# Optimization experiments

Hardware: AMD Instinct MI355X
Metric: run time of the kernel (lower is better)

Reference implementation:

```python
import jax, jax.numpy as jnp
import numpy as np

N_NODES = 50000
N_EDGES = 800000
F_IN = 128
HID = 128
F_EDGE = 16
F_TAB = 16
N_CLASSES = 3
BN_EPS = 1e-5


def setup_inputs() -> dict:
    key = jax.random.key(0)
    ks = jax.random.split(key, 20)
    s = lambda *sh: 1.0 / np.sqrt(sh[0])
    inp = {
        "x": jax.random.normal(ks[0], (N_NODES, F_IN), jnp.float32),
        "edge_index": jax.random.randint(ks[1], (2, N_EDGES), 0, N_NODES, jnp.int32),
        "edge_attr": jax.random.normal(ks[2], (N_EDGES, F_EDGE), jnp.float32),
        "tabular_features": jax.random.normal(ks[3], (N_EDGES, F_TAB), jnp.float32),
        # SAGEConv1: lin_l (aggregated neighbors, with bias) + lin_r (root, no bias)
        "W1l": jax.random.normal(ks[4], (F_IN, HID), jnp.float32) * s(F_IN),
        "b1l": jnp.zeros((HID,), jnp.float32),
        "W1r": jax.random.normal(ks[5], (F_IN, HID), jnp.float32) * s(F_IN),
        # SAGEConv2
        "W2l": jax.random.normal(ks[6], (HID, HID), jnp.float32) * s(HID),
        "b2l": jnp.zeros((HID,), jnp.float32),
        "W2r": jax.random.normal(ks[7], (HID, HID), jnp.float32) * s(HID),
        # BatchNorm params / running stats (eval mode)
        "g1": jnp.ones((HID,), jnp.float32), "be1": jnp.zeros((HID,), jnp.float32),
        "m1": jnp.zeros((HID,), jnp.float32), "v1": jnp.ones((HID,), jnp.float32),
        "g2": jnp.ones((HID,), jnp.float32), "be2": jnp.zeros((HID,), jnp.float32),
        "m2": jnp.zeros((HID,), jnp.float32), "v2": jnp.ones((HID,), jnp.float32),
        # Classifier MLP: (2*HID + F_EDGE + F_TAB) -> 128 -> 64 -> 3
        "Wc1": jax.random.normal(ks[8], (2 * HID + F_EDGE + F_TAB, 128), jnp.float32) * s(2 * HID + F_EDGE + F_TAB),
        "bc1": jnp.zeros((128,), jnp.float32),
        "Wc2": jax.random.normal(ks[9], (128, 64), jnp.float32) * s(128),
        "bc2": jnp.zeros((64,), jnp.float32),
        "Wc3": jax.random.normal(ks[10], (64, N_CLASSES), jnp.float32) * s(64),
        "bc3": jnp.zeros((N_CLASSES,), jnp.float32),
    }
    return inp


def _sage(x, src, dst, Wl, bl, Wr):
    # PyG SAGEConv (mean aggr): out_i = lin_l(mean_{j->i} x_j) + lin_r(x_i)
    msg = x[src]                                            # [E, F] gather
    agg = jax.ops.segment_sum(msg, dst, num_segments=N_NODES)
    cnt = jax.ops.segment_sum(jnp.ones((src.shape[0],), x.dtype), dst, num_segments=N_NODES)
    agg = agg / jnp.maximum(cnt, 1.0)[:, None]
    return agg @ Wl + bl + x @ Wr


def _bn(h, g, b, m, v):
    return (h - m) * (g * jax.lax.rsqrt(v + BN_EPS)) + b


def reference(x, edge_index, edge_attr, tabular_features,
              W1l, b1l, W1r, W2l, b2l, W2r,
              g1, be1, m1, v1, g2, be2, m2, v2,
              Wc1, bc1, Wc2, bc2, Wc3, bc3):
    src, dst = edge_index[0], edge_index[1]
    h = jax.nn.relu(_bn(_sage(x, src, dst, W1l, b1l, W1r), g1, be1, m1, v1))
    h = jax.nn.relu(_bn(_sage(h, src, dst, W2l, b2l, W2r), g2, be2, m2, v2))
    # eval mode: dropout is identity
    edge_repr = jnp.concatenate([h[src], h[dst], edge_attr, tabular_features], axis=-1)  # [E, 288]
    z = jax.nn.relu(edge_repr @ Wc1 + bc1)
    z = jax.nn.relu(z @ Wc2 + bc2)
    return z @ Wc3 + bc3  # [E, num_classes]
```

## Files before the change

### kernel.cpp

```cpp
#include <hip/hip_runtime.h>
#include <stdint.h>

#define NHID 128
#define EPB 64
#define RP  296
#define Z1P 136
#define Z2P 72

typedef _Float16 half8 __attribute__((ext_vector_type(8)));
typedef _Float16 half4v __attribute__((ext_vector_type(4)));
typedef float f32x4 __attribute__((ext_vector_type(4)));

__global__ void zero_kernel(float* __restrict__ p, size_t n4) {
    size_t i = (size_t)blockIdx.x * blockDim.x + threadIdx.x;
    size_t stride = (size_t)gridDim.x * blockDim.x;
    float4* p4 = (float4*)p;
    float4 z = make_float4(0.f, 0.f, 0.f, 0.f);
    for (size_t j = i; j < n4; j += stride) p4[j] = z;
}

__global__ void cast_f32_f16(const float* __restrict__ in, _Float16* __restrict__ outp,
                             int n8) {
    int i = blockIdx.x * 256 + threadIdx.x;
    int stride = gridDim.x * 256;
    for (int j = i; j < n8; j += stride) {
        float4 a = ((const float4*)in)[2 * j];
        float4 b = ((const float4*)in)[2 * j + 1];
        half8 v;
        v[0] = (_Float16)a.x; v[1] = (_Float16)a.y; v[2] = (_Float16)a.z; v[3] = (_Float16)a.w;
        v[4] = (_Float16)b.x; v[5] = (_Float16)b.y; v[6] = (_Float16)b.z; v[7] = (_Float16)b.w;
        ((half8*)outp)[j] = v;
    }
}

__global__ void prep_weights(const float* __restrict__ Wc1, const float* __restrict__ Wc2,
                             const float* __restrict__ Wc3,
                             const float* __restrict__ W1l, const float* __restrict__ W1r,
                             const float* __restrict__ W2l, const float* __restrict__ W2r,
                             _Float16* __restrict__ W1T, _Float16* __restrict__ W2T,
                             _Float16* __restrict__ W3T,
                             _Float16* __restrict__ WT1, _Float16* __restrict__ WT2) {
    int tid = blockIdx.x * 256 + threadIdx.x;
    if (tid < 288 * 128) {
        int n = tid / 288, k = tid % 288;
        W1T[tid] = (_Float16)Wc1[(size_t)k * 128 + n];
    }
    if (tid < 64 * 128) {
        int n = tid / 128, k = tid % 128;
        W2T[tid] = (_Float16)Wc2[(size_t)k * 64 + n];
    }
    if (tid < 16 * 64) {
        int n = tid / 64, k = tid % 64;
        W3T[tid] = (n < 3) ? (_Float16)Wc3[(size_t)k * 3 + n] : (_Float16)0.f;
    }
    if (tid < 128 * 256) {
        int n = tid / 256, k = tid % 256;
        WT1[tid] = (k < 128) ? (_Float16)W1l[(size_t)k * 128 + n]
                             : (_Float16)W1r[(size_t)(k - 128) * 128 + n];
        WT2[tid] = (k < 128) ? (_Float16)W2l[(size_t)k * 128 + n]
                             : (_Float16)W2r[(size_t)(k - 128) * 128 + n];
    }
}

__global__ void count_kernel(const int* __restrict__ dst, int* __restrict__ deg, int E) {
    int e = blockIdx.x * 256 + threadIdx.x;
    if (e < E) atomicAdd(&deg[dst[e]], 1);
}

__global__ __launch_bounds__(256) void csr_reduce(const int* __restrict__ deg,
                                                  int* __restrict__ bsum, int N) {
    __shared__ int b[256];
    int t = threadIdx.x;
    int i = blockIdx.x * 256 + t;
    int v = (i < N) ? deg[i] : 0;
    b[t] = v;
    __syncthreads();
#pragma unroll
    for (int off = 128; off > 0; off >>= 1) {
        if (t < off) b[t] += b[t + off];
        __syncthreads();
    }
    if (t == 0) bsum[blockIdx.x] = b[0];
}

__global__ __launch_bounds__(256) void csr_scan_partials(const int* __restrict__ bsum,
                                                         int* __restrict__ bpre,
                                                         int* __restrict__ rowptr,
                                                         int nb, int N) {
    __shared__ int b[256];
    int t = threadIdx.x;
    int v = (t < nb) ? bsum[t] : 0;
    b[t] = v;
    __syncthreads();
    int x = v;
#pragma unroll
    for (int off = 1; off < 256; off <<= 1) {
        int y = (t >= off) ? b[t - off] : 0;
        __syncthreads();
        x += y;
        b[t] = x;
        __syncthreads();
    }
    if (t < nb) bpre[t] = x - v;
    if (t == nb - 1) rowptr[N] = x;
}

__global__ __launch_bounds__(256) void csr_emit(const int* __restrict__ deg,
                                                const int* __restrict__ bpre,
                                                int* __restrict__ rowptr,
                                                int* __restrict__ cursor, int N) {
    __shared__ int b[256];
    int t = threadIdx.x;
    int i = blockIdx.x * 256 + t;
    int v = (i < N) ? deg[i] : 0;
    b[t] = v;
    __syncthreads();
    int x = v;
#pragma unroll
    for (int off = 1; off < 256; off <<= 1) {
        int y = (t >= off) ? b[t - off] : 0;
        __syncthreads();
        x += y;
        b[t] = x;
        __syncthreads();
    }
    if (i < N) {
        int excl = bpre[blockIdx.x] + x - v;
        rowptr[i] = excl;
        cursor[i] = excl;
    }
}

__global__ void fill_kernel(const int* __restrict__ src, const int* __restrict__ dst,
                            int* __restrict__ cursor, int* __restrict__ ssrc, int E) {
    int e = blockIdx.x * 256 + threadIdx.x;
    if (e < E) {
        int p = atomicAdd(&cursor[dst[e]], 1);
        ssrc[p] = src[e];
    }
}

__global__ __launch_bounds__(512) void sage_layer(
    const _Float16* __restrict__ xin, const int* __restrict__ rowptr,
    const int* __restrict__ ssrc,
    const _Float16* __restrict__ WT, const float* __restrict__ bl,
    const float* __restrict__ gam, const float* __restrict__ bet,
    const float* __restrict__ mu, const float* __restrict__ var,
    _Float16* __restrict__ outp, int N) {
    __shared__ _Float16 sAX[16][264];
    int tid = threadIdx.x;
    int node0 = blockIdx.x * 16;

    {
        int i = tid >> 5;
        int q = tid & 31;
        int node = node0 + i;
        int rs = rowptr[node], re = rowptr[node + 1];
        float4 acc = make_float4(0.f, 0.f, 0.f, 0.f);
        int e = rs;
        for (; e + 4 <= re; e += 4) {
            int s0 = ssrc[e], s1 = ssrc[e + 1], s2 = ssrc[e + 2], s3 = ssrc[e + 3];
            half4v v0 = *(const half4v*)&xin[(size_t)s0 * NHID + q * 4];
            half4v v1 = *(const half4v*)&xin[(size_t)s1 * NHID + q * 4];
            half4v v2 = *(const half4v*)&xin[(size_t)s2 * NHID + q * 4];
            half4v v3 = *(const half4v*)&xin[(size_t)s3 * NHID + q * 4];
            acc.x += ((float)v0[0] + (float)v1[0]) + ((float)v2[0] + (float)v3[0]);
            acc.y += ((float)v0[1] + (float)v1[1]) + ((float)v2[1] + (float)v3[1]);
            acc.z += ((float)v0[2] + (float)v1[2]) + ((float)v2[2] + (float)v3[2]);
            acc.w += ((float)v0[3] + (float)v1[3]) + ((float)v2[3] + (float)v3[3]);
        }
        for (; e < re; e++) {
            half4v v = *(const half4v*)&xin[(size_t)ssrc[e] * NHID + q * 4];
            acc.x += (float)v[0]; acc.y += (float)v[1];
            acc.z += (float)v[2]; acc.w += (float)v[3];
        }
        int deg = re - rs;
        float inv = (deg > 0) ? (1.0f / (float)deg) : 0.f;
        half4v av;
        av[0] = (_Float16)(acc.x * inv); av[1] = (_Float16)(acc.y * inv);
        av[2] = (_Float16)(acc.z * inv); av[3] = (_Float16)(acc.w * inv);
        *(half4v*)&sAX[i][q * 4] = av;
        *(half4v*)&sAX[i][128 + q * 4] = *(const half4v*)&xin[(size_t)node * NHID + q * 4];
    }
    __syncthreads();

    {
        int lane = tid & 63;
        int wave = tid >> 6;
        int l15 = lane & 15;
        int g = lane >> 4;
        const _Float16* wb = WT + (size_t)(wave * 16 + l15) * 256 + g * 8;
        f32x4 acc = (f32x4){0.f, 0.f, 0.f, 0.f};
#pragma unroll
        for (int kt = 0; kt < 8; kt++) {
            half8 af = *(const half8*)&sAX[l15][kt * 32 + g * 8];
            half8 bf = *(const half8*)(wb + kt * 32);
            acc = __builtin_amdgcn_mfma_f32_16x16x32_f16(af, bf, acc, 0, 0, 0);
        }
        int o = wave * 16 + l15;
        float scale = gam[o] * rsqrtf(var[o] + 1e-5f);
        float bias = bet[o];
        float mean = mu[o];
        float bb = bl[o];
#pragma unroll
        for (int r = 0; r < 4; r++) {
            float hv = acc[r] + bb;
            hv = (hv - mean) * scale + bias;
            hv = fmaxf(hv, 0.f);
            outp[(size_t)(node0 + g * 4 + r) * NHID + o] = (_Float16)hv;
        }
    }
}

__global__ __launch_bounds__(256, 1) void classifier_mfma(
    const _Float16* __restrict__ h2f, const int* __restrict__ src,
    const int* __restrict__ dst,
    const float* __restrict__ attr, const float* __restrict__ tab,
    const _Float16* __restrict__ W1T, const float* __restrict__ bc1,
    const _Float16* __restrict__ W2T, const float* __restrict__ bc2,
    const _Float16* __restrict__ W3T, const float* __restrict__ bc3,
    float* __restrict__ out, int E, int ntiles) {
    __shared__ _Float16 repr[EPB][RP];
    __shared__ _Float16 z1s[EPB][Z1P];
    _Float16* z2f = &repr[0][0];

    int tid = threadIdx.x;
    int lane = tid & 63;
    int wave = tid >> 6;
    int l15 = lane & 15;
    int g = lane >> 4;

    half8 B1[2][9];
#pragma unroll
    for (int nn = 0; nn < 2; nn++) {
        const _Float16* wb = W1T + (size_t)((2 * wave + nn) * 16 + l15) * 288 + g * 8;
#pragma unroll
        for (int kt = 0; kt < 9; kt++) B1[nn][kt] = *(const half8*)(wb + kt * 32);
    }
    float bias1[2];
#pragma unroll
    for (int nn = 0; nn < 2; nn++) bias1[nn] = bc1[(2 * wave + nn) * 16 + l15];
    half8 B2[4];
    const _Float16* w2base = W2T + (size_t)(wave * 16 + l15) * 128 + g * 8;
#pragma unroll
    for (int kt = 0; kt < 4; kt++) B2[kt] = *(const half8*)(w2base + kt * 32);
    float bias2 = bc2[wave * 16 + l15];
    half8 B3[2];
#pragma unroll
    for (int kt = 0; kt < 2; kt++)
        B3[kt] = *(const half8*)(W3T + (size_t)l15 * 64 + kt * 32 + g * 8);
    float bias3 = bc3[l15 < 3 ? l15 : 2];

    for (int t = blockIdx.x; t < ntiles; t += gridDim.x) {
        int e0 = t * EPB;
        {
            int el = tid >> 2, p = tid & 3;
            int e = e0 + el; if (e >= E) e = E - 1;
            int s = src[e], d = dst[e];
            const half8* hs = (const half8*)(h2f + (size_t)s * NHID + p * 32);
            const half8* hd = (const half8*)(h2f + (size_t)d * NHID + p * 32);
            half8* r = (half8*)&repr[el][0];
#pragma unroll
            for (int j = 0; j < 4; j++) r[p * 4 + j] = hs[j];
#pragma unroll
            for (int j = 0; j < 4; j++) r[16 + p * 4 + j] = hd[j];
            const float* ssrcp = (p < 2) ? (attr + (size_t)e * 16 + p * 8)
                                         : (tab + (size_t)e * 16 + (p - 2) * 8);
            int doff = (p < 2) ? (32 + p) : (34 + (p - 2));
            float4 a = ((const float4*)ssrcp)[0], b = ((const float4*)ssrcp)[1];
            half8 v;
            v[0] = (_Float16)a.x; v[1] = (_Float16)a.y; v[2] = (_Float16)a.z; v[3] = (_Float16)a.w;
            v[4] = (_Float16)b.x; v[5] = (_Float16)b.y; v[6] = (_Float16)b.z; v[7] = (_Float16)b.w;
            r[doff] = v;
        }
        __syncthreads();

#pragma unroll
        for (int at = 0; at < 4; at++) {
            const _Float16* ab = &repr[at * 16 + l15][g * 8];
            f32x4 acc0 = (f32x4){bias1[0], bias1[0], bias1[0], bias1[0]};
            f32x4 acc1 = (f32x4){bias1[1], bias1[1], bias1[1], bias1[1]};
#pragma unroll
            for (int kt = 0; kt < 9; kt++) {
                half8 af = *(const half8*)(ab + kt * 32);
                acc0 = __builtin_amdgcn_mfma_f32_16x16x32_f16(af, B1[0][kt], acc0, 0, 0, 0);
                acc1 = __builtin_amdgcn_mfma_f32_16x16x32_f16(af, B1[1][kt], acc1, 0, 0, 0);
            }
#pragma unroll
            for (int r = 0; r < 4; r++) {
                z1s[at * 16 + g * 4 + r][(2 * wave + 0) * 16 + l15] = (_Float16)fmaxf(acc0[r], 0.f);
                z1s[at * 16 + g * 4 + r][(2 * wave + 1) * 16 + l15] = (_Float16)fmaxf(acc1[r], 0.f);
            }
        }
        __syncthreads();

#pragma unroll
        for (int a = 0; a < 4; a++) {
            const _Float16* ab = &z1s[a * 16 + l15][g * 8];
            f32x4 acc2 = (f32x4){bias2, bias2, bias2, bias2};
#pragma unroll
            for (int kt = 0; kt < 4; kt++)
                acc2 = __builtin_amdgcn_mfma_f32_16x16x32_f16(*(const half8*)(ab + kt * 32),
                                                              B2[kt], acc2, 0, 0, 0);
#pragma unroll
            for (int r = 0; r < 4; r++)
                z2f[(size_t)(a * 16 + g * 4 + r) * Z2P + wave * 16 + l15] =
                    (_Float16)fmaxf(acc2[r], 0.f);
        }
        __syncthreads();

        {
            const _Float16* ab = z2f + (size_t)(wave * 16 + l15) * Z2P + g * 8;
            f32x4 acc3 = (f32x4){0.f, 0.f, 0.f, 0.f};
#pragma unroll
            for (int kt = 0; kt < 2; kt++)
                acc3 = __builtin_amdgcn_mfma_f32_16x16x32_f16(*(const half8*)(ab + kt * 32),
                                                              B3[kt], acc3, 0, 0, 0);
            if (l15 < 3) {
                int ebase = e0 + wave * 16 + g * 4;
#pragma unroll
                for (int r = 0; r < 4; r++) {
                    int e = ebase + r;
                    if (e < E) out[(size_t)e * 3 + l15] = acc3[r] + bias3;
                }
            }
        }
        __syncthreads();
    }
}

extern "C" void kernel_launch(void* const* d_in, const int* in_sizes, int n_in,
                              void* d_out, int out_size, void* d_ws, size_t ws_size,
                              hipStream_t stream) {
    const float* x    = (const float*)d_in[0];
    const int*   ei   = (const int*)d_in[1];
    const float* attr = (const float*)d_in[2];
    const float* tab  = (const float*)d_in[3];
    const float* W1l  = (const float*)d_in[4];
    const float* b1l  = (const float*)d_in[5];
    const float* W1r  = (const float*)d_in[6];
    const float* W2l  = (const float*)d_in[7];
    const float* b2l  = (const float*)d_in[8];
    const float* W2r  = (const float*)d_in[9];
    const float* g1   = (const float*)d_in[10];
    const float* be1  = (const float*)d_in[11];
    const float* m1   = (const float*)d_in[12];
    const float* v1   = (const float*)d_in[13];
    const float* g2   = (const float*)d_in[14];
    const float* be2  = (const float*)d_in[15];
    const float* m2   = (const float*)d_in[16];
    const float* v2   = (const float*)d_in[17];
    const float* Wc1  = (const float*)d_in[18];
    const float* bc1  = (const float*)d_in[19];
    const float* Wc2  = (const float*)d_in[20];
    const float* bc2  = (const float*)d_in[21];
    const float* Wc3  = (const float*)d_in[22];
    const float* bc3  = (const float*)d_in[23];
    float* out = (float*)d_out;

    const int N = in_sizes[0] / NHID;
    const int E = in_sizes[1] / 2;

    char* ws = (char*)d_ws;
    int*       rowptr = (int*)(ws + 0);
    int*       cursor = (int*)(ws + 204800);
    int*       deg    = (int*)(ws + 409600);
    int*       ssrc   = (int*)(ws + 614400);
    int*       bsum   = (int*)(ws + 3814400);
    int*       bpre   = (int*)(ws + 3815424);
    _Float16*  W1T    = (_Float16*)(ws + 3816448);
    _Float16*  W2T    = (_Float16*)(ws + 3890176);
    _Float16*  W3T    = (_Float16*)(ws + 3906560);
    _Float16*  WT1    = (_Float16*)(ws + 3908608);
    _Float16*  WT2    = (_Float16*)(ws + 3974144);
    _Float16*  xf     = (_Float16*)(ws + 4039680);
    _Float16*  h1f    = (_Float16*)(ws + 4039680 + (size_t)N * NHID * 2);
    _Float16*  h2f    = (_Float16*)(ws + 4039680 + 2 * (size_t)N * NHID * 2);

    const int* src = ei;
    const int* dst = ei + E;

    int eblocks = (E + 255) / 256;
    int cblocks = (N + 255) / 256;
    int nblocks16 = (N + 15) / 16;
    int ntiles  = (E + EPB - 1) / EPB;
    int cgrid   = ntiles < 2048 ? ntiles : 2048;
    int n8      = N * NHID / 8;

    prep_weights<<<144, 256, 0, stream>>>(Wc1, Wc2, Wc3, W1l, W1r, W2l, W2r,
                                          W1T, W2T, W3T, WT1, WT2);
    cast_f32_f16<<<1024, 256, 0, stream>>>(x, xf, n8);
    zero_kernel<<<16, 256, 0, stream>>>((float*)deg, 204800 / 16);
    count_kernel<<<eblocks, 256, 0, stream>>>(dst, deg, E);
    csr_reduce<<<cblocks, 256, 0, stream>>>(deg, bsum, N);
    csr_scan_partials<<<1, 256, 0, stream>>>(bsum, bpre, rowptr, cblocks, N);
    csr_emit<<<cblocks, 256, 0, stream>>>(deg, bpre, rowptr, cursor, N);
    fill_kernel<<<eblocks, 256, 0, stream>>>(src, dst, cursor, ssrc, E);
    sage_layer<<<nblocks16, 512, 0, stream>>>(xf, rowptr, ssrc, WT1, b1l,
                                              g1, be1, m1, v1, h1f, N);
    sage_layer<<<nblocks16, 512, 0, stream>>>(h1f, rowptr, ssrc, WT2, b2l,
                                              g2, be2, m2, v2, h2f, N);
    classifier_mfma<<<cgrid, 256, 0, stream>>>(h2f, src, dst, attr, tab,
                                               W1T, bc1, W2T, bc2, W3T, bc3,
                                               out, E, ntiles);
}
```

Before: 334.7 us.

## Prefetch next edge tile into registers and widen classifier to 512 threads

The classifier kernel now runs 512 threads per block over a persistent grid of 512 blocks. Each thread issues the gather loads (h2 rows for src and dst, edge attributes) for the next tile into registers while the MFMA stages of the current tile run, then writes them to shared memory at the top of the next iteration. Work for the two MLP layers is split across 8 waves by row and column tiles, and bias loads move from setup into the epilogues. This overlaps gather latency with compute, at the cost of more registers per thread and half the waves sitting idle in the final layer.

```diff
diff --git a/kernel.cpp b/kernel.cpp
--- a/kernel.cpp
+++ b/kernel.cpp
@@ -212,7 +212,7 @@
     }
 }
 
-__global__ __launch_bounds__(256, 1) void classifier_mfma(
+__global__ __launch_bounds__(512) void classifier_mfma(
     const _Float16* __restrict__ h2f, const int* __restrict__ src,
     const int* __restrict__ dst,
     const float* __restrict__ attr, const float* __restrict__ tab,
@@ -229,87 +229,115 @@
     int wave = tid >> 6;
     int l15 = lane & 15;
     int g = lane >> 4;
+    int sel = tid >> 3;
+    int sp = tid & 7;
+    int a0 = (wave & 1) * 2;
+    int n0 = (wave >> 1) * 2;
+    int nt2 = wave & 3;
+    int a20 = (wave >> 2) * 2;
 
     half8 B1[2][9];
 #pragma unroll
     for (int nn = 0; nn < 2; nn++) {
-        const _Float16* wb = W1T + (size_t)((2 * wave + nn) * 16 + l15) * 288 + g * 8;
+        const _Float16* wb = W1T + (size_t)((n0 + nn) * 16 + l15) * 288 + g * 8;
 #pragma unroll
         for (int kt = 0; kt < 9; kt++) B1[nn][kt] = *(const half8*)(wb + kt * 32);
     }
-    float bias1[2];
-#pragma unroll
-    for (int nn = 0; nn < 2; nn++) bias1[nn] = bc1[(2 * wave + nn) * 16 + l15];
     half8 B2[4];
-    const _Float16* w2base = W2T + (size_t)(wave * 16 + l15) * 128 + g * 8;
-#pragma unroll
-    for (int kt = 0; kt < 4; kt++) B2[kt] = *(const half8*)(w2base + kt * 32);
-    float bias2 = bc2[wave * 16 + l15];
+    {
+        const _Float16* wb = W2T + (size_t)(nt2 * 16 + l15) * 128 + g * 8;
+#pragma unroll
+        for (int kt = 0; kt < 4; kt++) B2[kt] = *(const half8*)(wb + kt * 32);
+    }
     half8 B3[2];
 #pragma unroll
     for (int kt = 0; kt < 2; kt++)
         B3[kt] = *(const half8*)(W3T + (size_t)l15 * 64 + kt * 32 + g * 8);
-    float bias3 = bc3[l15 < 3 ? l15 : 2];
-
-    for (int t = blockIdx.x; t < ntiles; t += gridDim.x) {
+
+    half8 shs0, shs1, shd0, shd1;
+    float4 sa0, sa1;
+
+    auto ISSUE = [&](int tp) {
+        int e = tp * EPB + sel; if (e >= E) e = E - 1;
+        int s = src[e], d = dst[e];
+        const half8* hs = (const half8*)(h2f + (size_t)s * NHID) + 2 * sp;
+        const half8* hd = (const half8*)(h2f + (size_t)d * NHID) + 2 * sp;
+        shs0 = hs[0]; shs1 = hs[1]; shd0 = hd[0]; shd1 = hd[1];
+        if (sp < 4) {
+            const float* ap = (sp < 2) ? (attr + (size_t)e * 16 + sp * 8)
+                                       : (tab + (size_t)e * 16 + (sp - 2) * 8);
+            sa0 = ((const float4*)ap)[0];
+            sa1 = ((const float4*)ap)[1];
+        }
+    };
+    auto WRITE = [&]() {
+        half8* r = (half8*)&repr[sel][0];
+        r[2 * sp] = shs0; r[2 * sp + 1] = shs1;
+        r[16 + 2 * sp] = shd0; r[16 + 2 * sp + 1] = shd1;
+        if (sp < 4) {
+            half8 v;
+            v[0] = (_Float16)sa0.x; v[1] = (_Float16)sa0.y;
+            v[2] = (_Float16)sa0.z; v[3] = (_Float16)sa0.w;
+            v[4] = (_Float16)sa1.x; v[5] = (_Float16)sa1.y;
+            v[6] = (_Float16)sa1.z; v[7] = (_Float16)sa1.w;
+            r[32 + sp] = v;
+        }
+    };
+
+    int gd = gridDim.x;
+    ISSUE(blockIdx.x);
+
+    for (int t = blockIdx.x; t < ntiles; t += gd) {
         int e0 = t * EPB;
+        WRITE();
+        __syncthreads();
+
         {
-            int el = tid >> 2, p = tid & 3;
-            int e = e0 + el; if (e >= E) e = E - 1;
-            int s = src[e], d = dst[e];
-            const half8* hs = (const half8*)(h2f + (size_t)s * NHID + p * 32);
-            const half8* hd = (const half8*)(h2f + (size_t)d * NHID + p * 32);
-            half8* r = (half8*)&repr[el][0];
-#pragma unroll
-            for (int j = 0; j < 4; j++) r[p * 4 + j] = hs[j];
-#pragma unroll
-            for (int j = 0; j < 4; j++) r[16 + p * 4 + j] = hd[j];
-            const float* ssrcp = (p < 2) ? (attr + (size_t)e * 16 + p * 8)
-                                         : (tab + (size_t)e * 16 + (p - 2) * 8);
-            int doff = (p < 2) ? (32 + p) : (34 + (p - 2));
-            float4 a = ((const float4*)ssrcp)[0], b = ((const float4*)ssrcp)[1];
-            half8 v;
-            v[0] = (_Float16)a.x; v[1] = (_Float16)a.y; v[2] = (_Float16)a.z; v[3] = (_Float16)a.w;
-            v[4] = (_Float16)b.x; v[5] = (_Float16)b.y; v[6] = (_Float16)b.z; v[7] = (_Float16)b.w;
-            r[doff] = v;
-        }
-        __syncthreads();
-
-#pragma unroll
-        for (int at = 0; at < 4; at++) {
-            const _Float16* ab = &repr[at * 16 + l15][g * 8];
-            f32x4 acc0 = (f32x4){bias1[0], bias1[0], bias1[0], bias1[0]};
-            f32x4 acc1 = (f32x4){bias1[1], bias1[1], bias1[1], bias1[1]};
+            int tp = t + gd; if (tp >= ntiles) tp = t;
+            ISSUE(tp);
+        }
+
+#pragma unroll
+        for (int aa = 0; aa < 2; aa++) {
+            const _Float16* ab = &repr[(a0 + aa) * 16 + l15][g * 8];
+            f32x4 acc0 = (f32x4){0.f, 0.f, 0.f, 0.f};
+            f32x4 acc1 = (f32x4){0.f, 0.f, 0.f, 0.f};
 #pragma unroll
             for (int kt = 0; kt < 9; kt++) {
                 half8 af = *(const half8*)(ab + kt * 32);
                 acc0 = __builtin_amdgcn_mfma_f32_16x16x32_f16(af, B1[0][kt], acc0, 0, 0, 0);
                 acc1 = __builtin_amdgcn_mfma_f32_16x16x32_f16(af, B1[1][kt], acc1, 0, 0, 0);
             }
+            float b1a = bc1[(n0 + 0) * 16 + l15];
+            float b1b = bc1[(n0 + 1) * 16 + l15];
 #pragma unroll
             for (int r = 0; r < 4; r++) {
-                z1s[at * 16 + g * 4 + r][(2 * wave + 0) * 16 + l15] = (_Float16)fmaxf(acc0[r], 0.f);
-                z1s[at * 16 + g * 4 + r][(2 * wave + 1) * 16 + l15] = (_Float16)fmaxf(acc1[r], 0.f);
+                z1s[(a0 + aa) * 16 + g * 4 + r][(n0 + 0) * 16 + l15] =
+                    (_Float16)fmaxf(acc0[r] + b1a, 0.f);
+                z1s[(a0 + aa) * 16 + g * 4 + r][(n0 + 1) * 16 + l15] =
+                    (_Float16)fmaxf(acc1[r] + b1b, 0.f);
             }
         }
         __syncthreads();
 
 #pragma unroll
-        for (int a = 0; a < 4; a++) {
-            const _Float16* ab = &z1s[a * 16 + l15][g * 8];
-            f32x4 acc2 = (f32x4){bias2, bias2, bias2, bias2};
+        for (int aa = 0; aa < 2; aa++) {
+            int at = a20 + aa;
+            const _Float16* ab = &z1s[at * 16 + l15][g * 8];
+            f32x4 acc2 = (f32x4){0.f, 0.f, 0.f, 0.f};
 #pragma unroll
             for (int kt = 0; kt < 4; kt++)
                 acc2 = __builtin_amdgcn_mfma_f32_16x16x32_f16(*(const half8*)(ab + kt * 32),
                                                               B2[kt], acc2, 0, 0, 0);
+            float b2 = bc2[nt2 * 16 + l15];
 #pragma unroll
             for (int r = 0; r < 4; r++)
-                z2f[(size_t)(a * 16 + g * 4 + r) * Z2P + wave * 16 + l15] =
-                    (_Float16)fmaxf(acc2[r], 0.f);
-        }
-        __syncthreads();
-
-        {
+                z2f[(size_t)(at * 16 + g * 4 + r) * Z2P + nt2 * 16 + l15] =
+                    (_Float16)fmaxf(acc2[r] + b2, 0.f);
+        }
+        __syncthreads();
+
+        if (wave < 4) {
             const _Float16* ab = z2f + (size_t)(wave * 16 + l15) * Z2P + g * 8;
             f32x4 acc3 = (f32x4){0.f, 0.f, 0.f, 0.f};
 #pragma unroll
@@ -317,11 +345,12 @@
                 acc3 = __builtin_amdgcn_mfma_f32_16x16x32_f16(*(const half8*)(ab + kt * 32),
                                                               B3[kt], acc3, 0, 0, 0);
             if (l15 < 3) {
+                float b3 = bc3[l15];
                 int ebase = e0 + wave * 16 + g * 4;
 #pragma unroll
                 for (int r = 0; r < 4; r++) {
                     int e = ebase + r;
-                    if (e < E) out[(size_t)e * 3 + l15] = acc3[r] + bias3;
+                    if (e < E) out[(size_t)e * 3 + l15] = acc3[r] + b3;
                 }
             }
         }
@@ -384,7 +413,8 @@
     int cblocks = (N + 255) / 256;
     int nblocks16 = (N + 15) / 16;
     int ntiles  = (E + EPB - 1) / EPB;
-    int cgrid   = ntiles < 2048 ? ntiles : 2048;
+    int cgrid   = 512;
+    if (cgrid > ntiles) cgrid = ntiles;
     int n8      = N * NHID / 8;
 
     prep_weights<<<144, 256, 0, stream>>>(Wc1, Wc2, Wc3, W1l, W1r, W2l, W2r,
@@ -400,7 +430,7 @@
                                               g1, be1, m1, v1, h1f, N);
     sage_layer<<<nblocks16, 512, 0, stream>>>(h1f, rowptr, ssrc, WT2, b2l,
                                               g2, be2, m2, v2, h2f, N);
-    classifier_mfma<<<cgrid, 256, 0, stream>>>(h2f, src, dst, attr, tab,
+    classifier_mfma<<<cgrid, 512, 0, stream>>>(h2f, src, dst, attr, tab,
                                                W1T, bc1, W2T, bc2, W3T, bc3,
                                                out, E, ntiles);
 }
```

Measured after the change: 376.2 us. 12.4% more time.
